# Performance work log

Measured on AMD Instinct MI355X. Metric: run time of the kernel, lower is better.

The kernel has to match this reference:

```python
import jax, jax.numpy as jnp
import numpy as np

STATE_DIM = 128
N_STATES = 4096
N_ACTIONS = 512
D = 16384  # random_feature_dim
B = 16     # batch of parallel episodes
ALPHA = 1.0
BETA = 1.0
SQRT_D = np.sqrt(D).astype(np.float32)


def _phi(W, x):
    """RandomFeatureMap: exp(1j * W @ x / alpha) / sqrt(D).
    W: [D, state_dim] real (torch randn .to(complex64) has zero imag part).
    x: [..., state_dim] real -> returns complex64 [..., D].
    """
    z = jnp.einsum('di,...i->...d', W, x) / ALPHA  # real phase
    return jax.lax.complex(jnp.cos(z), jnp.sin(z)) / SQRT_D


def setup_inputs() -> dict:
    key = jax.random.key(0)
    k1, k2, k3, k4, k5 = jax.random.split(key, 5)
    obs = jax.random.uniform(k1, (B, N_STATES), dtype=jnp.float32)
    action = jax.random.uniform(k2, (B, N_ACTIONS), dtype=jnp.float32)
    Q = jax.random.normal(k3, (STATE_DIM, N_STATES), dtype=jnp.float32) / np.sqrt(STATE_DIM).astype(np.float32)
    V = jax.random.normal(k4, (STATE_DIM, N_ACTIONS), dtype=jnp.float32) / np.sqrt(STATE_DIM).astype(np.float32)
    W = jax.random.normal(k5, (D, STATE_DIM), dtype=jnp.float32) / ALPHA
    return {"obs": obs, "action": action, "Q": Q, "V": V, "W": W}


def reference(obs, action, Q, V, W):
    # phi_Q = random_feature_map(Q.T).T : [D, n_states], also the memory M
    phi_Q = _phi(W, Q.T).T                                  # [D, S] complex64
    # get_state_from_memory: state = M @ obs
    state = phi_Q @ obs.T.astype(jnp.complex64)             # [D, B]
    # clean_up: weights = softmax(beta * Re(phi_Q^H @ state)); new_state = phi_Q @ weights
    scores = BETA * jnp.real(phi_Q.conj().T @ state)        # [S, B]
    weights = jax.nn.softmax(scores, axis=0)
    new_state = phi_Q @ weights.astype(jnp.complex64)       # [D, B]
    # update_state: state *= phi(V @ action)
    v = V @ action.T                                        # [state_dim, B]
    phi_v = _phi(W, v.T).T                                  # [D, B]
    out_state = new_state * phi_v
    # get_obs_from_memory: softmax(beta * Re(M^H @ state))
    out_scores = jax.nn.softmax(BETA * jnp.real(phi_Q.conj().T @ out_state), axis=0)  # [S, B]
    return out_scores
```

## Files before the change

kernel.cpp:

```cpp
#include <hip/hip_runtime.h>
#include <hip/hip_bf16.h>
#include <cstdint>
#include <cstddef>

#define D_DIM 16384
#define S_DIM 4096
#define A_DIM 512
#define K_DIM 128
#define B_DIM 16
#define CH    8

#define INV2PI 0.15915494309189535f

typedef float f32x4 __attribute__((ext_vector_type(4)));
typedef short s16x8 __attribute__((ext_vector_type(8)));
typedef unsigned short u16;
typedef unsigned int   u32;

__device__ __forceinline__ u16 bf16bits(float x) {
    return __builtin_bit_cast(u16, (__bf16)x);
}
__device__ __forceinline__ s16x8 frag_cast(uint4 u) {
    return __builtin_bit_cast(s16x8, u);
}
__device__ __forceinline__ u32 cvt_pk_bf16(float lo, float hi) {
    u32 r;
    asm("v_cvt_pk_bf16_f32 %0, %1, %2" : "=v"(r) : "v"(lo), "v"(hi));
    return r;
}
__device__ __forceinline__ int sigma(int row) {
    return (row & 7) ^ ((row >> 1) & 4);
}
__device__ __forceinline__ void g2l16(const u32* g, u32* l) {
    __builtin_amdgcn_global_load_lds((const __attribute__((address_space(1))) u32*)g,
                                     (__attribute__((address_space(3))) u32*)l, 16, 0, 0);
}

__global__ void prep_kernel(const float* __restrict__ W, const float* __restrict__ Q,
                            const float* __restrict__ obs,
                            u16* __restrict__ Wb, u16* __restrict__ QT, u16* __restrict__ obsP)
{
    const int i0 = blockIdx.x * 256 + threadIdx.x;
    const int stride = gridDim.x * 256;
    const float4* wp = (const float4*)W;
    for (int i = i0; i < D_DIM * 16; i += stride) {
        float4 a = wp[2 * i], b = wp[2 * i + 1];
        uint4 o;
        o.x = cvt_pk_bf16(a.x * INV2PI, a.y * INV2PI);
        o.y = cvt_pk_bf16(a.z * INV2PI, a.w * INV2PI);
        o.z = cvt_pk_bf16(b.x * INV2PI, b.y * INV2PI);
        o.w = cvt_pk_bf16(b.z * INV2PI, b.w * INV2PI);
        ((uint4*)Wb)[i] = o;
    }
    for (int i = i0; i < S_DIM * 16; i += stride) {
        const int s = i >> 4, kc = i & 15;
        float q[8];
        #pragma unroll
        for (int j = 0; j < 8; ++j) q[j] = Q[(size_t)(kc * 8 + j) * S_DIM + s];
        uint4 o;
        o.x = cvt_pk_bf16(q[0], q[1]);
        o.y = cvt_pk_bf16(q[2], q[3]);
        o.z = cvt_pk_bf16(q[4], q[5]);
        o.w = cvt_pk_bf16(q[6], q[7]);
        ((uint4*)QT)[s * 16 + kc] = o;
    }
    for (int i = i0; i < B_DIM * S_DIM; i += stride) {
        int b = i >> 12, s = i & 4095;
        obsP[((s >> 3) << 7) + (b << 3) + (s & 7)] = bf16bits(obs[i]);
    }
}

__global__ void kv_kernel(const float* __restrict__ V, const float* __restrict__ act,
                          float* __restrict__ v)
{
    const int t = threadIdx.x;
    const int out = blockIdx.x * 32 + (t >> 3);
    const int part = t & 7;
    const int k = out >> 4, b = out & 15;
    const float4* vp = (const float4*)(V + (size_t)k * A_DIM);
    const float4* ap = (const float4*)(act + (size_t)b * A_DIM);
    float s = 0.f;
    #pragma unroll
    for (int q = part * 16; q < part * 16 + 16; ++q) {
        float4 x = vp[q], y = ap[q];
        s += x.x * y.x + x.y * y.y + x.z * y.z + x.w * y.w;
    }
    s += __shfl_xor(s, 1, 64);
    s += __shfl_xor(s, 2, 64);
    s += __shfl_xor(s, 4, 64);
    if (part == 0) v[out] = s;
}

__global__ void phiv_kernel(const float* __restrict__ W, const float* __restrict__ v,
                            float* __restrict__ pvr, float* __restrict__ pvi)
{
    __shared__ float sv[K_DIM * 16];
    const int tid = threadIdx.x;
    for (int j = tid; j < K_DIM * 16; j += 256) sv[j] = v[j];
    __syncthreads();
    const int i = blockIdx.x * 256 + tid;
    const int d = i >> 4, b = i & 15;
    const float4* wp = (const float4*)(W + (size_t)d * K_DIM);
    float z = 0.f;
    #pragma unroll 8
    for (int q = 0; q < 32; ++q) {
        float4 w4 = wp[q];
        z += w4.x * sv[(4 * q + 0) * 16 + b] + w4.y * sv[(4 * q + 1) * 16 + b]
           + w4.z * sv[(4 * q + 2) * 16 + b] + w4.w * sv[(4 * q + 3) * 16 + b];
    }
    pvr[i] = cosf(z) * 0.0078125f;
    pvi[i] = sinf(z) * 0.0078125f;
}

template<int MODE>
__global__ __launch_bounds__(256, 2)
void fused_pass(const u16* __restrict__ P1, const u16* __restrict__ P2,
                const u16* __restrict__ y1, const u16* __restrict__ y2,
                float* __restrict__ out1, float* __restrict__ out2, int Mrows)
{
    __shared__ u32 lds[2][8192];
    const int tid = threadIdx.x;
    const int w   = tid >> 6;
    const int l   = tid & 63;
    const int n0  = l & 15;
    const int hi  = l >> 4;
    const int wm  = w & 1;
    const int wk  = w >> 1;
    const int m0  = blockIdx.x * 64 + wm * 32;
    const int kbase0 = blockIdx.y * (CH * 128);

    s16x8 bfrag[2][4];
    #pragma unroll
    for (int mt = 0; mt < 2; ++mt) {
        const uint4* ap = (const uint4*)(P1 + (size_t)(m0 + 16 * mt + n0) * 128);
        #pragma unroll
        for (int ki = 0; ki < 4; ++ki) bfrag[mt][ki] = frag_cast(ap[4 * ki + hi]);
    }

    int gofs[8];
    #pragma unroll
    for (int i = 0; i < 8; ++i) {
        const int row = 16 * i + (tid >> 4);
        gofs[i] = row * 128 + (((tid & 15) ^ sigma(row)) << 3);
    }
    const u16* p2base = P2 + (size_t)kbase0 * 128;

    f32x4 acc1[2] = {{0.f,0.f,0.f,0.f},{0.f,0.f,0.f,0.f}};
    f32x4 acc2[2] = {{0.f,0.f,0.f,0.f},{0.f,0.f,0.f,0.f}};

    const int rowperm = 8 * (n0 >> 2) + (n0 & 3);

    #pragma unroll
    for (int i = 0; i < 8; ++i)
        g2l16((const u32*)(p2base + gofs[i]), &lds[0][i * 1024 + w * 256]);
    __syncthreads();

    #pragma unroll 1
    for (int c = 0; c < CH; ++c) {
        if (c < CH - 1) {
            const u16* src = p2base + (size_t)(c + 1) * 128 * 128;
            #pragma unroll
            for (int i = 0; i < 8; ++i)
                g2l16((const u32*)(src + gofs[i]), &lds[(c + 1) & 1][i * 1024 + w * 256]);
        }
        const u32* buf = lds[c & 1];
        #pragma unroll
        for (int ks = 0; ks < 2; ++ks) {
            u32 cf0[4], sf0[4], cf1[4], sf1[4];
            #pragma unroll
            for (int T = 0; T < 2; ++T) {
                const int row = 64 * wk + 32 * ks + 4 * T + rowperm;
                const int sg  = sigma(row);
                const u32* rb = buf + row * 64;
                uint4 af[4];
                #pragma unroll
                for (int ki = 0; ki < 4; ++ki)
                    af[ki] = *(const uint4*)(rb + (((4 * ki + hi) ^ sg) << 2));
                f32x4 z0 = {0.f,0.f,0.f,0.f}, z1 = {0.f,0.f,0.f,0.f};
                #pragma unroll
                for (int ki = 0; ki < 4; ++ki) {
                    z0 = __builtin_amdgcn_mfma_f32_16x16x32_bf16(frag_cast(af[ki]), bfrag[0][ki], z0, 0, 0, 0);
                    z1 = __builtin_amdgcn_mfma_f32_16x16x32_bf16(frag_cast(af[ki]), bfrag[1][ki], z1, 0, 0, 0);
                }
                float c0[4], s0[4], c1[4], s1[4];
                #pragma unroll
                for (int r = 0; r < 4; ++r) {
                    const float rv0 = __builtin_amdgcn_fractf(z0[r]);
                    c0[r] = __builtin_amdgcn_cosf(rv0);
                    s0[r] = __builtin_amdgcn_sinf(rv0);
                    const float rv1 = __builtin_amdgcn_fractf(z1[r]);
                    c1[r] = __builtin_amdgcn_cosf(rv1);
                    s1[r] = __builtin_amdgcn_sinf(rv1);
                }
                cf0[2 * T + 0] = cvt_pk_bf16(c0[0], c0[1]);
                cf0[2 * T + 1] = cvt_pk_bf16(c0[2], c0[3]);
                sf0[2 * T + 0] = cvt_pk_bf16(s0[0], s0[1]);
                sf0[2 * T + 1] = cvt_pk_bf16(s0[2], s0[3]);
                cf1[2 * T + 0] = cvt_pk_bf16(c1[0], c1[1]);
                cf1[2 * T + 1] = cvt_pk_bf16(c1[2], c1[3]);
                sf1[2 * T + 0] = cvt_pk_bf16(s1[0], s1[1]);
                sf1[2 * T + 1] = cvt_pk_bf16(s1[2], s1[3]);
            }
            const s16x8 cfr0 = frag_cast(uint4{cf0[0], cf0[1], cf0[2], cf0[3]});
            const s16x8 sfr0 = frag_cast(uint4{sf0[0], sf0[1], sf0[2], sf0[3]});
            const s16x8 cfr1 = frag_cast(uint4{cf1[0], cf1[1], cf1[2], cf1[3]});
            const s16x8 sfr1 = frag_cast(uint4{sf1[0], sf1[1], sf1[2], sf1[3]});
            const size_t yg = (size_t)((kbase0 >> 3) + 16 * c + 8 * wk + 4 * ks + hi) * 128
                            + (size_t)n0 * 8;
            const s16x8 yf1 = frag_cast(*(const uint4*)(y1 + yg));
            if (MODE == 0) {
                acc1[0] = __builtin_amdgcn_mfma_f32_16x16x32_bf16(cfr0, yf1, acc1[0], 0, 0, 0);
                acc2[0] = __builtin_amdgcn_mfma_f32_16x16x32_bf16(sfr0, yf1, acc2[0], 0, 0, 0);
                acc1[1] = __builtin_amdgcn_mfma_f32_16x16x32_bf16(cfr1, yf1, acc1[1], 0, 0, 0);
                acc2[1] = __builtin_amdgcn_mfma_f32_16x16x32_bf16(sfr1, yf1, acc2[1], 0, 0, 0);
            } else {
                const s16x8 yf2 = frag_cast(*(const uint4*)(y2 + yg));
                acc1[0] = __builtin_amdgcn_mfma_f32_16x16x32_bf16(cfr0, yf1, acc1[0], 0, 0, 0);
                acc1[0] = __builtin_amdgcn_mfma_f32_16x16x32_bf16(sfr0, yf2, acc1[0], 0, 0, 0);
                acc1[1] = __builtin_amdgcn_mfma_f32_16x16x32_bf16(cfr1, yf1, acc1[1], 0, 0, 0);
                acc1[1] = __builtin_amdgcn_mfma_f32_16x16x32_bf16(sfr1, yf2, acc1[1], 0, 0, 0);
            }
        }
        __syncthreads();
    }

    float* red = reinterpret_cast<float*>(&lds[0][0]);
    if (wk == 1) {
        #pragma unroll
        for (int mt = 0; mt < 2; ++mt)
            #pragma unroll
            for (int r = 0; r < 4; ++r) {
                red[((wm * 2 + mt) * 16 + 4 * hi + r) * 16 + n0] = acc1[mt][r];
                if (MODE == 0)
                    red[1024 + ((wm * 2 + mt) * 16 + 4 * hi + r) * 16 + n0] = acc2[mt][r];
            }
    }
    __syncthreads();
    if (wk == 0) {
        float* o1 = out1 + (size_t)blockIdx.y * Mrows * 16;
        float* o2 = out2 + (size_t)blockIdx.y * Mrows * 16;
        #pragma unroll
        for (int mt = 0; mt < 2; ++mt)
            #pragma unroll
            for (int r = 0; r < 4; ++r) {
                const int orow = m0 + 16 * mt + 4 * hi + r;
                const float v1 = acc1[mt][r] + red[((wm * 2 + mt) * 16 + 4 * hi + r) * 16 + n0];
                if (MODE == 0) {
                    o1[orow * 16 + n0] = v1;
                    o2[orow * 16 + n0] = acc2[mt][r] + red[1024 + ((wm * 2 + mt) * 16 + 4 * hi + r) * 16 + n0];
                } else {
                    o1[(size_t)n0 * Mrows + orow] = v1;
                }
            }
    }
}

__global__ void finishA(const float* __restrict__ ar, const float* __restrict__ ai,
                        u16* __restrict__ pr, u16* __restrict__ pi)
{
    const int i = blockIdx.x * 256 + threadIdx.x;
    float sr = 0.f, si = 0.f;
    #pragma unroll
    for (int p = 0; p < 4; ++p) {
        sr += ar[(size_t)p * (D_DIM * 16) + i];
        si += ai[(size_t)p * (D_DIM * 16) + i];
    }
    const int d = i >> 4, b = i & 15;
    const int pidx = ((d >> 3) << 7) + (b << 3) + (d & 7);
    pr[pidx] = bf16bits(sr * 0.0078125f);
    pi[pidx] = bf16bits(si * 0.0078125f);
}

__global__ void finishC(const float* __restrict__ ar, const float* __restrict__ ai,
                        const float* __restrict__ pvr, const float* __restrict__ pvi,
                        u16* __restrict__ pr, u16* __restrict__ pi)
{
    const int i = blockIdx.x * 256 + threadIdx.x;
    float sr = 0.f, si = 0.f;
    #pragma unroll
    for (int p = 0; p < 4; ++p) {
        sr += ar[(size_t)p * (D_DIM * 16) + i];
        si += ai[(size_t)p * (D_DIM * 16) + i];
    }
    const float nr = sr * 0.0078125f, ni = si * 0.0078125f;
    const float xr = nr * pvr[i] - ni * pvi[i];
    const float xi = nr * pvi[i] + ni * pvr[i];
    const int d = i >> 4, b = i & 15;
    const int pidx = ((d >> 3) << 7) + (b << 3) + (d & 7);
    pr[pidx] = bf16bits(xr);
    pi[pidx] = bf16bits(xi);
}

template<int OUT>
__global__ void softmax_col(const float* __restrict__ acc, u16* __restrict__ wp,
                            float* __restrict__ outp)
{
    const int b = blockIdx.x;
    const int tid = threadIdx.x;
    __shared__ float red[4];
    float4 x[4];
    float m = -1e30f;
    #pragma unroll
    for (int j = 0; j < 4; ++j) {
        float4 s4 = {0.f, 0.f, 0.f, 0.f};
        #pragma unroll
        for (int p = 0; p < 16; ++p) {
            const float4 t = *(const float4*)(acc + (size_t)p * (S_DIM * 16)
                                              + (size_t)b * S_DIM + (j * 256 + tid) * 4);
            s4.x += t.x; s4.y += t.y; s4.z += t.z; s4.w += t.w;
        }
        x[j].x = s4.x * 0.0078125f; x[j].y = s4.y * 0.0078125f;
        x[j].z = s4.z * 0.0078125f; x[j].w = s4.w * 0.0078125f;
        m = fmaxf(fmaxf(m, fmaxf(x[j].x, x[j].y)), fmaxf(x[j].z, x[j].w));
    }
    #pragma unroll
    for (int off = 1; off < 64; off <<= 1) m = fmaxf(m, __shfl_xor(m, off, 64));
    if ((tid & 63) == 0) red[tid >> 6] = m;
    __syncthreads();
    m = fmaxf(fmaxf(red[0], red[1]), fmaxf(red[2], red[3]));
    float sum = 0.f;
    #pragma unroll
    for (int j = 0; j < 4; ++j) {
        x[j].x = expf(x[j].x - m); x[j].y = expf(x[j].y - m);
        x[j].z = expf(x[j].z - m); x[j].w = expf(x[j].w - m);
        sum += x[j].x + x[j].y + x[j].z + x[j].w;
    }
    #pragma unroll
    for (int off = 1; off < 64; off <<= 1) sum += __shfl_xor(sum, off, 64);
    __syncthreads();
    if ((tid & 63) == 0) red[tid >> 6] = sum;
    __syncthreads();
    const float inv = 1.0f / (red[0] + red[1] + red[2] + red[3]);
    #pragma unroll
    for (int j = 0; j < 4; ++j) {
        const int s4i = (j * 256 + tid) * 4;
        float v4[4] = {x[j].x * inv, x[j].y * inv, x[j].z * inv, x[j].w * inv};
        #pragma unroll
        for (int q = 0; q < 4; ++q) {
            const int s = s4i + q;
            if (OUT == 0) wp[((s >> 3) << 7) + (b << 3) + (s & 7)] = bf16bits(v4[q]);
            else          outp[s * 16 + b] = v4[q];
        }
    }
}

extern "C" void kernel_launch(void* const* d_in, const int* in_sizes, int n_in,
                              void* d_out, int out_size, void* d_ws, size_t ws_size,
                              hipStream_t stream)
{
    const float* obs = (const float*)d_in[0];
    const float* act = (const float*)d_in[1];
    const float* Q   = (const float*)d_in[2];
    const float* V   = (const float*)d_in[3];
    const float* W   = (const float*)d_in[4];
    float* out = (float*)d_out;
    char* ws = (char*)d_ws;

    u16*   Wb     = (u16*)  (ws + 0);
    u16*   QT     = (u16*)  (ws + 4194304);
    u16*   obsP   = (u16*)  (ws + 5242880);
    u16*   wP     = (u16*)  (ws + 5373952);
    u16*   stRe   = (u16*)  (ws + 5505024);
    u16*   stIm   = (u16*)  (ws + 6029312);
    u16*   osRe   = (u16*)  (ws + 6553600);
    u16*   osIm   = (u16*)  (ws + 7077888);
    float* pvR    = (float*)(ws + 7602176);
    float* pvI    = (float*)(ws + 8650752);
    float* vv     = (float*)(ws + 9699328);
    float* partR  = (float*)(ws + 9707520);
    float* partI  = (float*)(ws + 18096128);
    float* partS  = (float*)(ws + 9707520);

    prep_kernel<<<1024, 256, 0, stream>>>(W, Q, obs, Wb, QT, obsP);
    kv_kernel<<<64, 256, 0, stream>>>(V, act, vv);
    phiv_kernel<<<1024, 256, 0, stream>>>(W, vv, pvR, pvI);

    fused_pass<0><<<dim3(256, 4), 256, 0, stream>>>(Wb, QT, obsP, obsP, partR, partI, D_DIM);
    finishA<<<1024, 256, 0, stream>>>(partR, partI, stRe, stIm);

    fused_pass<1><<<dim3(64, 16), 256, 0, stream>>>(QT, Wb, stRe, stIm, partS, partS, S_DIM);
    softmax_col<0><<<16, 256, 0, stream>>>(partS, wP, nullptr);

    fused_pass<0><<<dim3(256, 4), 256, 0, stream>>>(Wb, QT, wP, wP, partR, partI, D_DIM);
    finishC<<<1024, 256, 0, stream>>>(partR, partI, pvR, pvI, osRe, osIm);

    fused_pass<1><<<dim3(64, 16), 256, 0, stream>>>(QT, Wb, osRe, osIm, partS, partS, S_DIM);
    softmax_col<1><<<16, 256, 0, stream>>>(partS, nullptr, out);
}
```

Measured before the change: 233.6 us.

## Deepen P2 staging to four-buffer pipeline with one barrier and prefetched y fragments

```diff
diff --git a/kernel.cpp b/kernel.cpp
--- a/kernel.cpp
+++ b/kernel.cpp
@@ -8,7 +8,7 @@
 #define A_DIM 512
 #define K_DIM 128
 #define B_DIM 16
-#define CH    8
+#define CH    16
 
 #define INV2PI 0.15915494309189535f
 
@@ -34,6 +34,9 @@
 __device__ __forceinline__ void g2l16(const u32* g, u32* l) {
     __builtin_amdgcn_global_load_lds((const __attribute__((address_space(1))) u32*)g,
                                      (__attribute__((address_space(3))) u32*)l, 16, 0, 0);
+}
+template<int N> __device__ __forceinline__ void vwait() {
+    asm volatile("s_waitcnt vmcnt(%0)" :: "n"(N) : "memory");
 }
 
 __global__ void prep_kernel(const float* __restrict__ W, const float* __restrict__ Q,
@@ -118,7 +121,7 @@
                 const u16* __restrict__ y1, const u16* __restrict__ y2,
                 float* __restrict__ out1, float* __restrict__ out2, int Mrows)
 {
-    __shared__ u32 lds[2][8192];
+    __shared__ u32 lds[4][4096];
     const int tid = threadIdx.x;
     const int w   = tid >> 6;
     const int l   = tid & 63;
@@ -127,7 +130,7 @@
     const int wm  = w & 1;
     const int wk  = w >> 1;
     const int m0  = blockIdx.x * 64 + wm * 32;
-    const int kbase0 = blockIdx.y * (CH * 128);
+    const int kbase0 = blockIdx.y * (CH * 64);
 
     s16x8 bfrag[2][4];
     #pragma unroll
@@ -137,92 +140,112 @@
         for (int ki = 0; ki < 4; ++ki) bfrag[mt][ki] = frag_cast(ap[4 * ki + hi]);
     }
 
-    int gofs[8];
-    #pragma unroll
-    for (int i = 0; i < 8; ++i) {
-        const int row = 16 * i + (tid >> 4);
-        gofs[i] = row * 128 + (((tid & 15) ^ sigma(row)) << 3);
+    int gofs[4];
+    #pragma unroll
+    for (int i = 0; i < 4; ++i) {
+        const int row = 16 * w + 4 * i + hi;
+        gofs[i] = row * 128 + ((n0 ^ sigma(row)) << 3);
     }
     const u16* p2base = P2 + (size_t)kbase0 * 128;
+
+    #define STAGE(c, b) { \
+        const u16* src_ = p2base + (size_t)(c) * 64 * 128; \
+        _Pragma("unroll") \
+        for (int i_ = 0; i_ < 4; ++i_) \
+            g2l16((const u32*)(src_ + gofs[i_]), &lds[b][w * 1024 + i_ * 256]); }
+
+    const size_t ybase = (size_t)(4 * wk + hi) * 128 + (size_t)n0 * 8;
+    #define YLD(Y, c) (*(const uint4*)((Y) + (size_t)((kbase0 + (c) * 64) >> 3) * 128 + ybase))
 
     f32x4 acc1[2] = {{0.f,0.f,0.f,0.f},{0.f,0.f,0.f,0.f}};
     f32x4 acc2[2] = {{0.f,0.f,0.f,0.f},{0.f,0.f,0.f,0.f}};
 
-    const int rowperm = 8 * (n0 >> 2) + (n0 & 3);
-
-    #pragma unroll
-    for (int i = 0; i < 8; ++i)
-        g2l16((const u32*)(p2base + gofs[i]), &lds[0][i * 1024 + w * 256]);
-    __syncthreads();
+    const int rowT0 = 32 * wk + 8 * (n0 >> 2) + (n0 & 3);
+
+    STAGE(0, 0);
+    uint4 y1c = YLD(y1, 0);
+    uint4 y2c;
+    if (MODE == 1) y2c = YLD(y2, 0);
+    STAGE(1, 1);
 
     #pragma unroll 1
     for (int c = 0; c < CH; ++c) {
+        uint4 y1n, y2n;
         if (c < CH - 1) {
-            const u16* src = p2base + (size_t)(c + 1) * 128 * 128;
+            y1n = YLD(y1, c + 1);
+            if (MODE == 1) y2n = YLD(y2, c + 1);
+        }
+        if (c < CH - 2) {
+            STAGE(c + 2, (c + 2) & 3);
+            vwait<8 + ((MODE == 1) ? 2 : 1)>();
+        } else if (c == CH - 2) {
+            vwait<4 + ((MODE == 1) ? 2 : 1)>();
+        } else {
+            vwait<0>();
+        }
+        __builtin_amdgcn_s_barrier();
+        __builtin_amdgcn_sched_barrier(0);
+
+        const u32* buf = lds[c & 3];
+        u32 cf0[4], sf0[4], cf1[4], sf1[4];
+        #pragma unroll
+        for (int T = 0; T < 2; ++T) {
+            const int row = rowT0 + 4 * T;
+            const int sg  = sigma(row);
+            const u32* rb = buf + row * 64;
+            uint4 af[4];
             #pragma unroll
-            for (int i = 0; i < 8; ++i)
-                g2l16((const u32*)(src + gofs[i]), &lds[(c + 1) & 1][i * 1024 + w * 256]);
-        }
-        const u32* buf = lds[c & 1];
-        #pragma unroll
-        for (int ks = 0; ks < 2; ++ks) {
-            u32 cf0[4], sf0[4], cf1[4], sf1[4];
+            for (int ki = 0; ki < 4; ++ki)
+                af[ki] = *(const uint4*)(rb + (((4 * ki + hi) ^ sg) << 2));
+            f32x4 z0 = {0.f,0.f,0.f,0.f}, z1 = {0.f,0.f,0.f,0.f};
             #pragma unroll
-            for (int T = 0; T < 2; ++T) {
-                const int row = 64 * wk + 32 * ks + 4 * T + rowperm;
-                const int sg  = sigma(row);
-                const u32* rb = buf + row * 64;
-                uint4 af[4];
-                #pragma unroll
-                for (int ki = 0; ki < 4; ++ki)
-                    af[ki] = *(const uint4*)(rb + (((4 * ki + hi) ^ sg) << 2));
-                f32x4 z0 = {0.f,0.f,0.f,0.f}, z1 = {0.f,0.f,0.f,0.f};
-                #pragma unroll
-                for (int ki = 0; ki < 4; ++ki) {
-                    z0 = __builtin_amdgcn_mfma_f32_16x16x32_bf16(frag_cast(af[ki]), bfrag[0][ki], z0, 0, 0, 0);
-                    z1 = __builtin_amdgcn_mfma_f32_16x16x32_bf16(frag_cast(af[ki]), bfrag[1][ki], z1, 0, 0, 0);
-                }
-                float c0[4], s0[4], c1[4], s1[4];
-                #pragma unroll
-                for (int r = 0; r < 4; ++r) {
-                    const float rv0 = __builtin_amdgcn_fractf(z0[r]);
-                    c0[r] = __builtin_amdgcn_cosf(rv0);
-                    s0[r] = __builtin_amdgcn_sinf(rv0);
-                    const float rv1 = __builtin_amdgcn_fractf(z1[r]);
-                    c1[r] = __builtin_amdgcn_cosf(rv1);
-                    s1[r] = __builtin_amdgcn_sinf(rv1);
-                }
-                cf0[2 * T + 0] = cvt_pk_bf16(c0[0], c0[1]);
-                cf0[2 * T + 1] = cvt_pk_bf16(c0[2], c0[3]);
-                sf0[2 * T + 0] = cvt_pk_bf16(s0[0], s0[1]);
-                sf0[2 * T + 1] = cvt_pk_bf16(s0[2], s0[3]);
-                cf1[2 * T + 0] = cvt_pk_bf16(c1[0], c1[1]);
-                cf1[2 * T + 1] = cvt_pk_bf16(c1[2], c1[3]);
-                sf1[2 * T + 0] = cvt_pk_bf16(s1[0], s1[1]);
-                sf1[2 * T + 1] = cvt_pk_bf16(s1[2], s1[3]);
+            for (int ki = 0; ki < 4; ++ki) {
+                z0 = __builtin_amdgcn_mfma_f32_16x16x32_bf16(frag_cast(af[ki]), bfrag[0][ki], z0, 0, 0, 0);
+                z1 = __builtin_amdgcn_mfma_f32_16x16x32_bf16(frag_cast(af[ki]), bfrag[1][ki], z1, 0, 0, 0);
             }
-            const s16x8 cfr0 = frag_cast(uint4{cf0[0], cf0[1], cf0[2], cf0[3]});
-            const s16x8 sfr0 = frag_cast(uint4{sf0[0], sf0[1], sf0[2], sf0[3]});
-            const s16x8 cfr1 = frag_cast(uint4{cf1[0], cf1[1], cf1[2], cf1[3]});
-            const s16x8 sfr1 = frag_cast(uint4{sf1[0], sf1[1], sf1[2], sf1[3]});
-            const size_t yg = (size_t)((kbase0 >> 3) + 16 * c + 8 * wk + 4 * ks + hi) * 128
-                            + (size_t)n0 * 8;
-            const s16x8 yf1 = frag_cast(*(const uint4*)(y1 + yg));
-            if (MODE == 0) {
-                acc1[0] = __builtin_amdgcn_mfma_f32_16x16x32_bf16(cfr0, yf1, acc1[0], 0, 0, 0);
-                acc2[0] = __builtin_amdgcn_mfma_f32_16x16x32_bf16(sfr0, yf1, acc2[0], 0, 0, 0);
-                acc1[1] = __builtin_amdgcn_mfma_f32_16x16x32_bf16(cfr1, yf1, acc1[1], 0, 0, 0);
-                acc2[1] = __builtin_amdgcn_mfma_f32_16x16x32_bf16(sfr1, yf1, acc2[1], 0, 0, 0);
-            } else {
-                const s16x8 yf2 = frag_cast(*(const uint4*)(y2 + yg));
-                acc1[0] = __builtin_amdgcn_mfma_f32_16x16x32_bf16(cfr0, yf1, acc1[0], 0, 0, 0);
-                acc1[0] = __builtin_amdgcn_mfma_f32_16x16x32_bf16(sfr0, yf2, acc1[0], 0, 0, 0);
-                acc1[1] = __builtin_amdgcn_mfma_f32_16x16x32_bf16(cfr1, yf1, acc1[1], 0, 0, 0);
-                acc1[1] = __builtin_amdgcn_mfma_f32_16x16x32_bf16(sfr1, yf2, acc1[1], 0, 0, 0);
+            float c0[4], s0[4], c1[4], s1[4];
+            #pragma unroll
+            for (int r = 0; r < 4; ++r) {
+                const float rv0 = __builtin_amdgcn_fractf(z0[r]);
+                c0[r] = __builtin_amdgcn_cosf(rv0);
+                s0[r] = __builtin_amdgcn_sinf(rv0);
+                const float rv1 = __builtin_amdgcn_fractf(z1[r]);
+                c1[r] = __builtin_amdgcn_cosf(rv1);
+                s1[r] = __builtin_amdgcn_sinf(rv1);
             }
-        }
-        __syncthreads();
-    }
+            cf0[2 * T + 0] = cvt_pk_bf16(c0[0], c0[1]);
+            cf0[2 * T + 1] = cvt_pk_bf16(c0[2], c0[3]);
+            sf0[2 * T + 0] = cvt_pk_bf16(s0[0], s0[1]);
+            sf0[2 * T + 1] = cvt_pk_bf16(s0[2], s0[3]);
+            cf1[2 * T + 0] = cvt_pk_bf16(c1[0], c1[1]);
+            cf1[2 * T + 1] = cvt_pk_bf16(c1[2], c1[3]);
+            sf1[2 * T + 0] = cvt_pk_bf16(s1[0], s1[1]);
+            sf1[2 * T + 1] = cvt_pk_bf16(s1[2], s1[3]);
+        }
+        const s16x8 cfr0 = frag_cast(uint4{cf0[0], cf0[1], cf0[2], cf0[3]});
+        const s16x8 sfr0 = frag_cast(uint4{sf0[0], sf0[1], sf0[2], sf0[3]});
+        const s16x8 cfr1 = frag_cast(uint4{cf1[0], cf1[1], cf1[2], cf1[3]});
+        const s16x8 sfr1 = frag_cast(uint4{sf1[0], sf1[1], sf1[2], sf1[3]});
+        const s16x8 yf1 = frag_cast(y1c);
+        if (MODE == 0) {
+            acc1[0] = __builtin_amdgcn_mfma_f32_16x16x32_bf16(cfr0, yf1, acc1[0], 0, 0, 0);
+            acc2[0] = __builtin_amdgcn_mfma_f32_16x16x32_bf16(sfr0, yf1, acc2[0], 0, 0, 0);
+            acc1[1] = __builtin_amdgcn_mfma_f32_16x16x32_bf16(cfr1, yf1, acc1[1], 0, 0, 0);
+            acc2[1] = __builtin_amdgcn_mfma_f32_16x16x32_bf16(sfr1, yf1, acc2[1], 0, 0, 0);
+        } else {
+            const s16x8 yf2 = frag_cast(y2c);
+            acc1[0] = __builtin_amdgcn_mfma_f32_16x16x32_bf16(cfr0, yf1, acc1[0], 0, 0, 0);
+            acc1[0] = __builtin_amdgcn_mfma_f32_16x16x32_bf16(sfr0, yf2, acc1[0], 0, 0, 0);
+            acc1[1] = __builtin_amdgcn_mfma_f32_16x16x32_bf16(cfr1, yf1, acc1[1], 0, 0, 0);
+            acc1[1] = __builtin_amdgcn_mfma_f32_16x16x32_bf16(sfr1, yf2, acc1[1], 0, 0, 0);
+        }
+        if (c < CH - 1) {
+            y1c = y1n;
+            if (MODE == 1) y2c = y2n;
+        }
+    }
+    #undef STAGE
+    #undef YLD
 
     float* red = reinterpret_cast<float*>(&lds[0][0]);
     if (wk == 1) {
```

Result: slower. 242.5 us (+3.8%).
